# Optimization experiments

Measured on AMD Instinct MI355X. Metric: run time of the kernel, lower is better.

The kernel has to match this reference:

```python
import jax, jax.numpy as jnp
import numpy as np

B, L, H = 2, 2048, 1024
N_HEADS = 16
HEAD = H // N_HEADS
LN_EPS = 1e-12


def setup_inputs() -> dict:
    key = jax.random.key(0)
    ks = jax.random.split(key, 8)
    s = 1.0 / np.sqrt(H)
    return {
        "embeddings": jax.random.normal(ks[0], (B, L, H), dtype=jnp.float32),
        "mask": jnp.zeros((B, 1, 1, L), dtype=jnp.float32),
        "Wq": jax.random.normal(ks[1], (H, H), dtype=jnp.float32) * s,
        "bq": jnp.zeros((H,), dtype=jnp.float32),
        "Wk": jax.random.normal(ks[2], (H, H), dtype=jnp.float32) * s,
        "bk": jnp.zeros((H,), dtype=jnp.float32),
        "Wv": jax.random.normal(ks[3], (H, H), dtype=jnp.float32) * s,
        "bv": jnp.zeros((H,), dtype=jnp.float32),
        "Wo": jax.random.normal(ks[4], (H, H), dtype=jnp.float32) * s,
        "bo": jnp.zeros((H,), dtype=jnp.float32),
        "ln_gamma": jnp.ones((H,), dtype=jnp.float32),
        "ln_beta": jnp.zeros((H,), dtype=jnp.float32),
    }


def _layer_norm(x, gamma, beta):
    mu = jnp.mean(x, axis=-1, keepdims=True)
    var = jnp.mean(jnp.square(x - mu), axis=-1, keepdims=True)
    return (x - mu) * jax.lax.rsqrt(var + LN_EPS) * gamma + beta


def reference(embeddings, mask, Wq, bq, Wk, bk, Wv, bv, Wo, bo, ln_gamma, ln_beta):
    b, l, h = embeddings.shape
    # QKV projections, split heads -> [b, n_heads, l, head]
    def split_heads(x):
        return x.reshape(b, l, N_HEADS, HEAD).transpose(0, 2, 1, 3)
    q = split_heads(embeddings @ Wq + bq)
    k = split_heads(embeddings @ Wk + bk)
    v = split_heads(embeddings @ Wv + bv)
    # Faithful to source: energies use Q @ V^T, scaled by sqrt(n_heads)
    energies = jnp.einsum("bhqd,bhkd->bhqk", q, v) / np.sqrt(N_HEADS) + mask
    weights = jax.nn.softmax(energies, axis=3)
    # Faithful to source: attended = weights @ K
    attended = jnp.einsum("bhqk,bhkd->bhqd", weights, k)
    attended = attended.transpose(0, 2, 1, 3).reshape(b, l, h)
    # Residual feed-forward (BertSelfOutput style): dense + residual + LN
    out = attended @ Wo + bo
    return _layer_norm(out + embeddings, ln_gamma, ln_beta)
```

## Files before the change

### kernel.cpp

```cpp
#include <hip/hip_runtime.h>

#define LOG2E 1.44269504f
#define C_QSCALE 0.360673760f
#define C_SHIFT  34.6246810f
typedef unsigned short u16;
typedef short bf16x8 __attribute__((ext_vector_type(8)));
typedef float f32x4 __attribute__((ext_vector_type(4)));
typedef unsigned short u16x4 __attribute__((ext_vector_type(4)));

#define BB 2
#define LL 2048
#define HH 1024
#define NH 16
#define HD 64
#define ML (BB*LL)

__device__ __forceinline__ u16 f2bf(float f) {
  union { float f; unsigned u; } v; v.f = f;
  unsigned r = v.u + 0x7FFFu + ((v.u >> 16) & 1u);
  return (u16)(r >> 16);
}
__device__ __forceinline__ u16 f2bf_trunc(float f) {
  union { float f; unsigned u; } v; v.f = f;
  return (u16)(v.u >> 16);
}
__device__ __forceinline__ void gload_lds16(const u16* g, u16* l) {
  __builtin_amdgcn_global_load_lds((const __attribute__((address_space(1))) void*)g,
                                   (__attribute__((address_space(3))) void*)l, 16, 0, 0);
}

__global__ __launch_bounds__(256) void k_prep(const float* __restrict__ E, u16* __restrict__ X,
                                              const float* W0, const float* W1,
                                              const float* W2, const float* W3,
                                              u16* __restrict__ WT) {
  __shared__ __align__(16) u16 T[64*72];
  if (blockIdx.x < 2048) {
    int idx = (blockIdx.x * 256 + threadIdx.x) * 8;
    float4 a = *(const float4*)(E + idx);
    float4 b = *(const float4*)(E + idx + 4);
    bf16x8 o;
    o[0]=f2bf(a.x); o[1]=f2bf(a.y); o[2]=f2bf(a.z); o[3]=f2bf(a.w);
    o[4]=f2bf(b.x); o[5]=f2bf(b.y); o[6]=f2bf(b.z); o[7]=f2bf(b.w);
    *(bf16x8*)(X + idx) = o;
    return;
  }
  int bz = blockIdx.x - 2048;
  int z = bz >> 8, rem = bz & 255, bx = rem & 15, by = rem >> 4;
  const float* W = (z==0)?W0:(z==1)?W1:(z==2)?W2:W3;
  u16* dst = WT + (size_t)z * HH * HH;
  int t = threadIdx.x;
  int n0 = bx * 64, k0 = by * 64;
  int kl = t >> 2, nc = t & 3;
  #pragma unroll
  for (int u = 0; u < 4; ++u) {
    float4 v = *(const float4*)(W + (size_t)(k0 + kl) * HH + n0 + nc*16 + u*4);
    int nb = nc*16 + u*4;
    T[(nb+0)*72 + kl] = f2bf(v.x);
    T[(nb+1)*72 + kl] = f2bf(v.y);
    T[(nb+2)*72 + kl] = f2bf(v.z);
    T[(nb+3)*72 + kl] = f2bf(v.w);
  }
  __syncthreads();
  int nl = t >> 2, kc = (t & 3) * 16;
  #pragma unroll
  for (int e = 0; e < 2; ++e) {
    bf16x8 v = *(const bf16x8*)(T + nl*72 + kc + e*8);
    *(bf16x8*)(dst + (size_t)(n0+nl)*HH + k0 + kc + e*8) = v;
  }
}

__global__ __launch_bounds__(256) void k_gemm(const u16* __restrict__ A, const u16* __restrict__ Bt,
                                              const float* __restrict__ b0, const float* __restrict__ b1,
                                              const float* __restrict__ b2,
                                              u16* __restrict__ QH, u16* __restrict__ KV,
                                              float* __restrict__ outf, int mode) {
  __shared__ __align__(16) u16 As[2][128*32];
  __shared__ __align__(16) u16 Bs[2][128*32];
  int tid = threadIdx.x;
  int lane = tid & 63, w = tid >> 6;
  int c = lane & 15, g = lane >> 4;
  int bn0 = blockIdx.x * 128, bm0 = blockIdx.y * 128;
  int wm0 = (w >> 1) * 64, wn0 = (w & 1) * 64;
  int z = bn0 >> 10;
  bool swapd = (mode == 1) || (z != 1);
  const u16* srcA = swapd ? Bt : A;
  const u16* srcB = swapd ? A : Bt;
  int baseA = swapd ? bn0 : bm0;
  int baseB = swapd ? bm0 : bn0;

  f32x4 acc[4][4];
  #pragma unroll
  for (int mt = 0; mt < 4; ++mt)
    #pragma unroll
    for (int nt = 0; nt < 4; ++nt)
      acc[mt][nt] = (f32x4){0.f,0.f,0.f,0.f};

  #pragma unroll
  for (int it = 0; it < 2; ++it) {
    int ch = tid + it*256, row = ch >> 2, col = (ch & 3) * 8;
    gload_lds16(srcA + (size_t)(baseA + row) * HH + col, &As[0][ch*8]);
    gload_lds16(srcB + (size_t)(baseB + row) * HH + col, &Bs[0][ch*8]);
  }
  for (int kt = 0; kt < 32; ++kt) {
    __syncthreads();
    int cb = kt & 1;
    if (kt < 31) {
      int k0 = (kt + 1) * 32, nb = (kt + 1) & 1;
      #pragma unroll
      for (int it = 0; it < 2; ++it) {
        int ch = tid + it*256, row = ch >> 2, col = (ch & 3) * 8;
        gload_lds16(srcA + (size_t)(baseA + row) * HH + k0 + col, &As[nb][ch*8]);
        gload_lds16(srcB + (size_t)(baseB + row) * HH + k0 + col, &Bs[nb][ch*8]);
      }
    }
    bf16x8 af[4], bfr[4];
    #pragma unroll
    for (int i = 0; i < 4; ++i) {
      af[i]  = *(const bf16x8*)(&As[cb][0] + (wm0 + i*16 + c)*32 + g*8);
      bfr[i] = *(const bf16x8*)(&Bs[cb][0] + (wn0 + i*16 + c)*32 + g*8);
    }
    #pragma unroll
    for (int mt = 0; mt < 4; ++mt)
      #pragma unroll
      for (int nt = 0; nt < 4; ++nt)
        acc[mt][nt] = __builtin_amdgcn_mfma_f32_16x16x32_bf16(af[mt], bfr[nt], acc[mt][nt], 0, 0, 0);
  }

  if (mode == 1) {
    #pragma unroll
    for (int mt = 0; mt < 4; ++mt) {
      int n0 = bn0 + wm0 + mt*16 + 4*g;
      float4 bv = *(const float4*)(b0 + n0);
      #pragma unroll
      for (int nt = 0; nt < 4; ++nt) {
        int tok = bm0 + wn0 + nt*16 + c;
        float4 o;
        o.x = acc[mt][nt][0] + bv.x;
        o.y = acc[mt][nt][1] + bv.y;
        o.z = acc[mt][nt][2] + bv.z;
        o.w = acc[mt][nt][3] + bv.w;
        *(float4*)(outf + (size_t)tok * HH + n0) = o;
      }
    }
  } else if (z == 1) {
    #pragma unroll
    for (int nt = 0; nt < 4; ++nt) {
      int n = bn0 + wn0 + nt*16 + c;
      int nn = n & 1023, h = nn >> 6, d = nn & 63;
      float bv = b1[nn];
      #pragma unroll
      for (int mt = 0; mt < 4; ++mt) {
        int m0 = bm0 + wm0 + mt*16 + 4*g;
        int b = m0 >> 11, keyl = m0 & 2047;
        int tt = keyl >> 6, chunk = (keyl >> 3) & 7, s = keyl & 7;
        u16x4 pk;
        #pragma unroll
        for (int r = 0; r < 4; ++r) pk[r] = f2bf(acc[mt][nt][r] + bv);
        *(u16x4*)(KV + ((size_t)((b*NH + h)*32 + tt))*8192 + d*64 + ((chunk ^ (d & 7))*8) + s) = pk;
      }
    }
  } else {
    #pragma unroll
    for (int mt = 0; mt < 4; ++mt) {
      int nidx0 = bn0 + wm0 + mt*16 + 4*g;
      int nn0 = nidx0 & 1023, h = nn0 >> 6, d0 = nn0 & 63;
      const float* bp = (z == 0) ? b0 : b2;
      float4 bv = *(const float4*)(bp + nn0);
      #pragma unroll
      for (int nt = 0; nt < 4; ++nt) {
        int tok = bm0 + wn0 + nt*16 + c;
        int b = tok >> 11, l = tok & 2047;
        u16x4 o;
        o[0] = f2bf(acc[mt][nt][0] + bv.x);
        o[1] = f2bf(acc[mt][nt][1] + bv.y);
        o[2] = f2bf(acc[mt][nt][2] + bv.z);
        o[3] = f2bf(acc[mt][nt][3] + bv.w);
        if (z == 0) {
          *(u16x4*)(QH + (((size_t)(b*NH + h)) * LL + l) * HD + d0) = o;
        } else {
          int tt = l >> 6;
          *(u16x4*)(KV + ((size_t)((b*NH + h)*32 + tt))*8192 + 4096
                    + (l & 63)*64 + (((d0 >> 3) ^ (l & 7))*8) + (d0 & 7)) = o;
        }
      }
    }
  }
}

__global__ __launch_bounds__(256) void k_attn(const u16* __restrict__ QH, const u16* __restrict__ KV,
                                              const float* __restrict__ mask, u16* __restrict__ ATT) {
  __shared__ __align__(16) u16 sKV[2][8192];
  __shared__ __align__(16) u16 sP[4][16*72];
  int tid = threadIdx.x;
  int lane = tid & 63, w = tid >> 6;
  int c = lane & 15, g = lane >> 4;
  int bh = blockIdx.y, b = bh >> 4, h = bh & 15;
  int q0 = blockIdx.x * 64 + w * 16;
  size_t qbase = (size_t)bh * LL * HD;
  const u16* kvg = KV + (size_t)bh * 32 * 8192;
  const float* mptr = mask + b * LL;

  bf16x8 aq[2];
  aq[0] = *(const bf16x8*)(QH + qbase + (size_t)(q0 + c) * HD + g*8);
  aq[1] = *(const bf16x8*)(QH + qbase + (size_t)(q0 + c) * HD + 32 + g*8);

  bf16x8 ones;
  #pragma unroll
  for (int i = 0; i < 8; ++i) ones[i] = (short)0x3F80;

  f32x4 O[4], lac;
  lac = (f32x4){0.f,0.f,0.f,0.f};
  #pragma unroll
  for (int dt = 0; dt < 4; ++dt) O[dt] = (f32x4){0.f,0.f,0.f,0.f};
  u16* pw = &sP[w][0];

  #pragma unroll
  for (int it = 0; it < 4; ++it) {
    int i = (tid + it*256) * 8;
    gload_lds16(kvg + i, &sKV[0][0] + i);
  }
  for (int t = 0; t < 32; ++t) {
    __syncthreads();
    const u16* cur = &sKV[t & 1][0];
    if (t < 31) {
      const u16* src = kvg + (size_t)(t + 1) * 8192;
      u16* dst = &sKV[(t + 1) & 1][0];
      #pragma unroll
      for (int it = 0; it < 4; ++it) {
        int i = (tid + it*256) * 8;
        gload_lds16(src + i, dst + i);
      }
    }
    int kv0 = t * 64;
    #pragma unroll
    for (int nt = 0; nt < 4; ++nt) {
      int vrow = nt*16 + c;
      bf16x8 vb0 = *(const bf16x8*)(cur + 4096 + vrow*64 + ((g ^ (c & 7))*8));
      bf16x8 vb1 = *(const bf16x8*)(cur + 4096 + vrow*64 + (((4 + g) ^ (c & 7))*8));
      float mterm = fmaf(mptr[kv0 + vrow], LOG2E, -C_SHIFT);
      f32x4 sa = (f32x4){0.f,0.f,0.f,0.f};
      sa = __builtin_amdgcn_mfma_f32_16x16x32_bf16(aq[0], vb0, sa, 0,0,0);
      sa = __builtin_amdgcn_mfma_f32_16x16x32_bf16(aq[1], vb1, sa, 0,0,0);
      #pragma unroll
      for (int r = 0; r < 4; ++r)
        pw[(4*g + r)*72 + nt*16 + c] = f2bf_trunc(exp2f(fmaf(sa[r], C_QSCALE, mterm)));
    }
    bf16x8 ap0 = *(const bf16x8*)(pw + c*72 + g*8);
    bf16x8 ap1 = *(const bf16x8*)(pw + c*72 + 32 + g*8);
    lac = __builtin_amdgcn_mfma_f32_16x16x32_bf16(ones, ap0, lac, 0,0,0);
    lac = __builtin_amdgcn_mfma_f32_16x16x32_bf16(ones, ap1, lac, 0,0,0);
    #pragma unroll
    for (int dt = 0; dt < 4; ++dt) {
      int d = dt*16 + c;
      bf16x8 bk0 = *(const bf16x8*)(cur + d*64 + ((g ^ (c & 7))*8));
      bf16x8 bk1 = *(const bf16x8*)(cur + d*64 + (((4 + g) ^ (c & 7))*8));
      O[dt] = __builtin_amdgcn_mfma_f32_16x16x32_bf16(bk0, ap0, O[dt], 0,0,0);
      O[dt] = __builtin_amdgcn_mfma_f32_16x16x32_bf16(bk1, ap1, O[dt], 0,0,0);
    }
  }
  float inv = 1.0f / lac[0];
  size_t orow = ((size_t)(b*LL + q0 + c)) * HH + h*HD;
  #pragma unroll
  for (int dt = 0; dt < 4; ++dt) {
    u16x4 o;
    #pragma unroll
    for (int r = 0; r < 4; ++r) o[r] = f2bf(O[dt][r] * inv);
    *(u16x4*)(ATT + orow + dt*16 + 4*g) = o;
  }
}

__global__ __launch_bounds__(256) void k_ln(const float* __restrict__ OF, const float* __restrict__ E,
                                            const float* __restrict__ gamma, const float* __restrict__ beta,
                                            float* __restrict__ out) {
  int row = blockIdx.x;
  int tid = threadIdx.x, lane = tid & 63, w = tid >> 6;
  size_t basei = (size_t)row * HH + tid*4;
  float4 a = *(const float4*)(OF + basei);
  float4 e = *(const float4*)(E + basei);
  float x0 = a.x + e.x, x1 = a.y + e.y, x2 = a.z + e.z, x3 = a.w + e.w;
  float s1 = x0+x1+x2+x3;
  float s2 = x0*x0+x1*x1+x2*x2+x3*x3;
  #pragma unroll
  for (int off = 32; off; off >>= 1) { s1 += __shfl_xor(s1, off); s2 += __shfl_xor(s2, off); }
  __shared__ float r1[4], r2[4];
  if (lane == 0) { r1[w] = s1; r2[w] = s2; }
  __syncthreads();
  s1 = r1[0]+r1[1]+r1[2]+r1[3];
  s2 = r2[0]+r2[1]+r2[2]+r2[3];
  float mu = s1 * (1.0f/HH);
  float var = s2 * (1.0f/HH) - mu*mu;
  float rs = rsqrtf(fmaxf(var, 0.f) + 1e-12f);
  int colb = tid*4;
  float4 gm = *(const float4*)(gamma + colb);
  float4 bt = *(const float4*)(beta + colb);
  float4 o;
  o.x = (x0-mu)*rs*gm.x + bt.x;
  o.y = (x1-mu)*rs*gm.y + bt.y;
  o.z = (x2-mu)*rs*gm.z + bt.z;
  o.w = (x3-mu)*rs*gm.w + bt.w;
  *(float4*)(out + basei) = o;
}

extern "C" void kernel_launch(void* const* d_in, const int* in_sizes, int n_in,
                              void* d_out, int out_size, void* d_ws, size_t ws_size,
                              hipStream_t stream) {
  const float* E    = (const float*)d_in[0];
  const float* mask = (const float*)d_in[1];
  const float* Wq   = (const float*)d_in[2];
  const float* bq   = (const float*)d_in[3];
  const float* Wk   = (const float*)d_in[4];
  const float* bk   = (const float*)d_in[5];
  const float* Wv   = (const float*)d_in[6];
  const float* bv   = (const float*)d_in[7];
  const float* Wo   = (const float*)d_in[8];
  const float* bo   = (const float*)d_in[9];
  const float* gam  = (const float*)d_in[10];
  const float* bet  = (const float*)d_in[11];

  const size_t MH = (size_t)ML * HH;
  u16* XBF = (u16*)d_ws;
  u16* WT  = XBF + MH;
  u16* QH  = WT + 4*(size_t)HH*HH;
  u16* KV  = QH + MH;
  u16* ATT = KV + 2*MH;
  float* OF = (float*)QH;
  float* out = (float*)d_out;

  k_prep<<<dim3(3072), 256, 0, stream>>>(E, XBF, Wq, Wk, Wv, Wo, WT);
  k_gemm<<<dim3(24,32), 256, 0, stream>>>(XBF, WT, bq, bk, bv, QH, KV, nullptr, 0);
  k_attn<<<dim3(32,32), 256, 0, stream>>>(QH, KV, mask, ATT);
  k_gemm<<<dim3(8,32), 256, 0, stream>>>(ATT, WT + 3*(size_t)HH*HH, bo, nullptr, nullptr,
                                         nullptr, nullptr, OF, 1);
  k_ln<<<dim3(ML), 256, 0, stream>>>(OF, E, gam, bet, out);
}
```

Measured before the change: 271.8 us.

## Restructure attention: split KV range across wave halves, read K/V directly from global

The attention kernel drops the LDS double-buffered K/V staging. Each wave now handles 32 queries instead of 16, and the 2048-key range is split between two halves of a 512-thread block, with partial outputs and row sums combined through shared memory at the end. The QKV GEMM epilogue writes K transposed in plain 64x64 tiles and V in head-major layout without the XOR swizzle, so the B-operand fragments can be loaded straight from global/L2. This targets LDS traffic and barriers in the inner loop and doubles MFMA reuse of each K/V fragment. The cost is heavier reliance on cache for the repeated global loads, plus an extra cross-wave reduction step.

Result: slower. 309.7 us (+14.0%).

```diff
diff --git a/kernel.cpp b/kernel.cpp
--- a/kernel.cpp
+++ b/kernel.cpp
@@ -72,7 +72,8 @@
 __global__ __launch_bounds__(256) void k_gemm(const u16* __restrict__ A, const u16* __restrict__ Bt,
                                               const float* __restrict__ b0, const float* __restrict__ b1,
                                               const float* __restrict__ b2,
-                                              u16* __restrict__ QH, u16* __restrict__ KV,
+                                              u16* __restrict__ QH, u16* __restrict__ KT,
+                                              u16* __restrict__ VHp,
                                               float* __restrict__ outf, int mode) {
   __shared__ __align__(16) u16 As[2][128*32];
   __shared__ __align__(16) u16 Bs[2][128*32];
@@ -152,19 +153,20 @@
       for (int mt = 0; mt < 4; ++mt) {
         int m0 = bm0 + wm0 + mt*16 + 4*g;
         int b = m0 >> 11, keyl = m0 & 2047;
-        int tt = keyl >> 6, chunk = (keyl >> 3) & 7, s = keyl & 7;
+        int tt = keyl >> 6;
         u16x4 pk;
         #pragma unroll
         for (int r = 0; r < 4; ++r) pk[r] = f2bf(acc[mt][nt][r] + bv);
-        *(u16x4*)(KV + ((size_t)((b*NH + h)*32 + tt))*8192 + d*64 + ((chunk ^ (d & 7))*8) + s) = pk;
+        *(u16x4*)(KT + ((size_t)((b*NH + h)*32 + tt))*4096 + d*64 + (keyl & 63)) = pk;
       }
     }
   } else {
+    u16* dst = (z == 0) ? QH : VHp;
+    const float* bp = (z == 0) ? b0 : b2;
     #pragma unroll
     for (int mt = 0; mt < 4; ++mt) {
       int nidx0 = bn0 + wm0 + mt*16 + 4*g;
       int nn0 = nidx0 & 1023, h = nn0 >> 6, d0 = nn0 & 63;
-      const float* bp = (z == 0) ? b0 : b2;
       float4 bv = *(const float4*)(bp + nn0);
       #pragma unroll
       for (int nt = 0; nt < 4; ++nt) {
@@ -175,97 +177,115 @@
         o[1] = f2bf(acc[mt][nt][1] + bv.y);
         o[2] = f2bf(acc[mt][nt][2] + bv.z);
         o[3] = f2bf(acc[mt][nt][3] + bv.w);
-        if (z == 0) {
-          *(u16x4*)(QH + (((size_t)(b*NH + h)) * LL + l) * HD + d0) = o;
-        } else {
-          int tt = l >> 6;
-          *(u16x4*)(KV + ((size_t)((b*NH + h)*32 + tt))*8192 + 4096
-                    + (l & 63)*64 + (((d0 >> 3) ^ (l & 7))*8) + (d0 & 7)) = o;
-        }
-      }
-    }
-  }
-}
-
-__global__ __launch_bounds__(256) void k_attn(const u16* __restrict__ QH, const u16* __restrict__ KV,
-                                              const float* __restrict__ mask, u16* __restrict__ ATT) {
-  __shared__ __align__(16) u16 sKV[2][8192];
-  __shared__ __align__(16) u16 sP[4][16*72];
+        *(u16x4*)(dst + (((size_t)(b*NH + h)) * LL + l) * HD + d0) = o;
+      }
+    }
+  }
+}
+
+__global__ __launch_bounds__(512, 4) void k_attn(const u16* __restrict__ QH, const u16* __restrict__ KT,
+                                                 const u16* __restrict__ VHp,
+                                                 const float* __restrict__ mask, u16* __restrict__ ATT) {
+  __shared__ __align__(16) char smem[36864];
   int tid = threadIdx.x;
   int lane = tid & 63, w = tid >> 6;
   int c = lane & 15, g = lane >> 4;
+  int unit = w & 3, half = w >> 2;
   int bh = blockIdx.y, b = bh >> 4, h = bh & 15;
-  int q0 = blockIdx.x * 64 + w * 16;
-  size_t qbase = (size_t)bh * LL * HD;
-  const u16* kvg = KV + (size_t)bh * 32 * 8192;
+  int q0 = (blockIdx.x * 4 + unit) * 32;
+  size_t base = (size_t)bh * LL * HD;
+  const u16* ktb = KT + (size_t)bh * 32 * 4096;
   const float* mptr = mask + b * LL;
-
-  bf16x8 aq[2];
-  aq[0] = *(const bf16x8*)(QH + qbase + (size_t)(q0 + c) * HD + g*8);
-  aq[1] = *(const bf16x8*)(QH + qbase + (size_t)(q0 + c) * HD + 32 + g*8);
+  u16* pw = (u16*)smem + w * 2304;
+
+  bf16x8 aq[2][2];
+  #pragma unroll
+  for (int qi = 0; qi < 2; ++qi)
+    #pragma unroll
+    for (int ks = 0; ks < 2; ++ks)
+      aq[qi][ks] = *(const bf16x8*)(QH + base + (size_t)(q0 + qi*16 + c) * HD + ks*32 + g*8);
 
   bf16x8 ones;
   #pragma unroll
   for (int i = 0; i < 8; ++i) ones[i] = (short)0x3F80;
 
-  f32x4 O[4], lac;
-  lac = (f32x4){0.f,0.f,0.f,0.f};
-  #pragma unroll
-  for (int dt = 0; dt < 4; ++dt) O[dt] = (f32x4){0.f,0.f,0.f,0.f};
-  u16* pw = &sP[w][0];
-
-  #pragma unroll
-  for (int it = 0; it < 4; ++it) {
-    int i = (tid + it*256) * 8;
-    gload_lds16(kvg + i, &sKV[0][0] + i);
-  }
-  for (int t = 0; t < 32; ++t) {
-    __syncthreads();
-    const u16* cur = &sKV[t & 1][0];
-    if (t < 31) {
-      const u16* src = kvg + (size_t)(t + 1) * 8192;
-      u16* dst = &sKV[(t + 1) & 1][0];
-      #pragma unroll
-      for (int it = 0; it < 4; ++it) {
-        int i = (tid + it*256) * 8;
-        gload_lds16(src + i, dst + i);
-      }
-    }
-    int kv0 = t * 64;
+  f32x4 O[2][4], lac[2];
+  #pragma unroll
+  for (int qi = 0; qi < 2; ++qi) {
+    lac[qi] = (f32x4){0.f,0.f,0.f,0.f};
+    #pragma unroll
+    for (int dt = 0; dt < 4; ++dt) O[qi][dt] = (f32x4){0.f,0.f,0.f,0.f};
+  }
+
+  int t0 = half * 16;
+  for (int tt = 0; tt < 16; ++tt) {
+    int t = t0 + tt, kv0 = t * 64;
     #pragma unroll
     for (int nt = 0; nt < 4; ++nt) {
-      int vrow = nt*16 + c;
-      bf16x8 vb0 = *(const bf16x8*)(cur + 4096 + vrow*64 + ((g ^ (c & 7))*8));
-      bf16x8 vb1 = *(const bf16x8*)(cur + 4096 + vrow*64 + (((4 + g) ^ (c & 7))*8));
-      float mterm = fmaf(mptr[kv0 + vrow], LOG2E, -C_SHIFT);
-      f32x4 sa = (f32x4){0.f,0.f,0.f,0.f};
-      sa = __builtin_amdgcn_mfma_f32_16x16x32_bf16(aq[0], vb0, sa, 0,0,0);
-      sa = __builtin_amdgcn_mfma_f32_16x16x32_bf16(aq[1], vb1, sa, 0,0,0);
-      #pragma unroll
-      for (int r = 0; r < 4; ++r)
-        pw[(4*g + r)*72 + nt*16 + c] = f2bf_trunc(exp2f(fmaf(sa[r], C_QSCALE, mterm)));
-    }
-    bf16x8 ap0 = *(const bf16x8*)(pw + c*72 + g*8);
-    bf16x8 ap1 = *(const bf16x8*)(pw + c*72 + 32 + g*8);
-    lac = __builtin_amdgcn_mfma_f32_16x16x32_bf16(ones, ap0, lac, 0,0,0);
-    lac = __builtin_amdgcn_mfma_f32_16x16x32_bf16(ones, ap1, lac, 0,0,0);
+      int vrow = kv0 + nt*16 + c;
+      const u16* vp = VHp + base + (size_t)vrow * HD + g*8;
+      bf16x8 vb0 = *(const bf16x8*)(vp);
+      bf16x8 vb1 = *(const bf16x8*)(vp + 32);
+      float mterm = fmaf(mptr[vrow], LOG2E, -C_SHIFT);
+      #pragma unroll
+      for (int qi = 0; qi < 2; ++qi) {
+        f32x4 sa = (f32x4){0.f,0.f,0.f,0.f};
+        sa = __builtin_amdgcn_mfma_f32_16x16x32_bf16(aq[qi][0], vb0, sa, 0,0,0);
+        sa = __builtin_amdgcn_mfma_f32_16x16x32_bf16(aq[qi][1], vb1, sa, 0,0,0);
+        #pragma unroll
+        for (int r = 0; r < 4; ++r)
+          pw[(qi*16 + 4*g + r)*72 + nt*16 + c] = f2bf_trunc(exp2f(fmaf(sa[r], C_QSCALE, mterm)));
+      }
+    }
+    bf16x8 ap[2][2];
+    #pragma unroll
+    for (int qi = 0; qi < 2; ++qi) {
+      ap[qi][0] = *(const bf16x8*)(pw + (qi*16 + c)*72 + g*8);
+      ap[qi][1] = *(const bf16x8*)(pw + (qi*16 + c)*72 + 32 + g*8);
+      lac[qi] = __builtin_amdgcn_mfma_f32_16x16x32_bf16(ones, ap[qi][0], lac[qi], 0,0,0);
+      lac[qi] = __builtin_amdgcn_mfma_f32_16x16x32_bf16(ones, ap[qi][1], lac[qi], 0,0,0);
+    }
     #pragma unroll
     for (int dt = 0; dt < 4; ++dt) {
       int d = dt*16 + c;
-      bf16x8 bk0 = *(const bf16x8*)(cur + d*64 + ((g ^ (c & 7))*8));
-      bf16x8 bk1 = *(const bf16x8*)(cur + d*64 + (((4 + g) ^ (c & 7))*8));
-      O[dt] = __builtin_amdgcn_mfma_f32_16x16x32_bf16(bk0, ap0, O[dt], 0,0,0);
-      O[dt] = __builtin_amdgcn_mfma_f32_16x16x32_bf16(bk1, ap1, O[dt], 0,0,0);
-    }
-  }
-  float inv = 1.0f / lac[0];
-  size_t orow = ((size_t)(b*LL + q0 + c)) * HH + h*HD;
-  #pragma unroll
-  for (int dt = 0; dt < 4; ++dt) {
-    u16x4 o;
-    #pragma unroll
-    for (int r = 0; r < 4; ++r) o[r] = f2bf(O[dt][r] * inv);
-    *(u16x4*)(ATT + orow + dt*16 + 4*g) = o;
+      const u16* kp = ktb + (size_t)t*4096 + d*64 + g*8;
+      bf16x8 bk0 = *(const bf16x8*)(kp);
+      bf16x8 bk1 = *(const bf16x8*)(kp + 32);
+      #pragma unroll
+      for (int qi = 0; qi < 2; ++qi) {
+        O[qi][dt] = __builtin_amdgcn_mfma_f32_16x16x32_bf16(bk0, ap[qi][0], O[qi][dt], 0,0,0);
+        O[qi][dt] = __builtin_amdgcn_mfma_f32_16x16x32_bf16(bk1, ap[qi][1], O[qi][dt], 0,0,0);
+      }
+    }
+  }
+
+  __syncthreads();
+  float* su = (float*)smem + (size_t)unit * 2176;
+  if (half == 1) {
+    #pragma unroll
+    for (int qi = 0; qi < 2; ++qi) {
+      #pragma unroll
+      for (int dt = 0; dt < 4; ++dt)
+        *(f32x4*)(su + (qi*16 + c)*68 + dt*16 + 4*g) = O[qi][dt];
+      if (g == 0) su[(qi*16 + c)*68 + 64] = lac[qi][0];
+    }
+  }
+  __syncthreads();
+  if (half == 0) {
+    #pragma unroll
+    for (int qi = 0; qi < 2; ++qi) {
+      float l = lac[qi][0] + su[(qi*16 + c)*68 + 64];
+      float inv = 1.0f / l;
+      size_t orow = ((size_t)(b*LL + q0 + qi*16 + c)) * HH + h*HD;
+      #pragma unroll
+      for (int dt = 0; dt < 4; ++dt) {
+        f32x4 po = *(const f32x4*)(su + (qi*16 + c)*68 + dt*16 + 4*g);
+        u16x4 o;
+        #pragma unroll
+        for (int r = 0; r < 4; ++r) o[r] = f2bf((O[qi][dt][r] + po[r]) * inv);
+        *(u16x4*)(ATT + orow + dt*16 + 4*g) = o;
+      }
+    }
   }
 }
 
@@ -321,15 +341,16 @@
   u16* XBF = (u16*)d_ws;
   u16* WT  = XBF + MH;
   u16* QH  = WT + 4*(size_t)HH*HH;
-  u16* KV  = QH + MH;
-  u16* ATT = KV + 2*MH;
+  u16* KT  = QH + MH;
+  u16* VHp = KT + MH;
+  u16* ATT = VHp + MH;
   float* OF = (float*)QH;
   float* out = (float*)d_out;
 
   k_prep<<<dim3(3072), 256, 0, stream>>>(E, XBF, Wq, Wk, Wv, Wo, WT);
-  k_gemm<<<dim3(24,32), 256, 0, stream>>>(XBF, WT, bq, bk, bv, QH, KV, nullptr, 0);
-  k_attn<<<dim3(32,32), 256, 0, stream>>>(QH, KV, mask, ATT);
+  k_gemm<<<dim3(24,32), 256, 0, stream>>>(XBF, WT, bq, bk, bv, QH, KT, VHp, nullptr, 0);
+  k_attn<<<dim3(16,32), 512, 0, stream>>>(QH, KT, VHp, mask, ATT);
   k_gemm<<<dim3(8,32), 256, 0, stream>>>(ATT, WT + 3*(size_t)HH*HH, bo, nullptr, nullptr,
-                                         nullptr, nullptr, OF, 1);
+                                         nullptr, nullptr, nullptr, OF, 1);
   k_ln<<<dim3(ML), 256, 0, stream>>>(OF, E, gam, bet, out);
 }
```
